# Optimization experiments

Hardware: AMD Instinct MI355X
Metric: run time of the kernel (lower is better)

The kernel has to match this reference:

```python
import jax, jax.numpy as jnp
import numpy as np

B = 64
H_FS = W_FS = 56
IN_DIM, OUT_DIM, NUM_HEADS = 96, 192, 2
HEAD_DIM = OUT_DIM // NUM_HEADS  # 96
STRIDE_Q, STRIDE_KV = (2, 2), (4, 4)
REL_RANGE = 2 * (H_FS // STRIDE_Q[0]) - 1  # 55
LN_EPS = 1e-5


def setup_inputs() -> dict:
    key = jax.random.key(0)
    ks = jax.random.split(key, 12)
    N = H_FS * W_FS + 1  # +1 cls token
    s = 0.02
    d = {
        "hidden_states": jax.random.normal(ks[0], (B, N, IN_DIM), jnp.float32),
        "Wq": jax.random.normal(ks[1], (IN_DIM, OUT_DIM), jnp.float32) * s,
        "bq": jnp.zeros((OUT_DIM,), jnp.float32),
        "Wk": jax.random.normal(ks[2], (IN_DIM, OUT_DIM), jnp.float32) * s,
        "bk": jnp.zeros((OUT_DIM,), jnp.float32),
        "Wv": jax.random.normal(ks[3], (IN_DIM, OUT_DIM), jnp.float32) * s,
        "bv": jnp.zeros((OUT_DIM,), jnp.float32),
        # depthwise pool convs: (C_out=C, C_in/groups=1, kh, kw)
        "pool_q_w": jax.random.normal(ks[4], (IN_DIM, 1, 3, 3), jnp.float32) * 0.1,
        "pool_k_w": jax.random.normal(ks[5], (IN_DIM, 1, 3, 3), jnp.float32) * 0.1,
        "pool_v_w": jax.random.normal(ks[6], (IN_DIM, 1, 3, 3), jnp.float32) * 0.1,
        "gq": jnp.ones((IN_DIM,), jnp.float32), "betaq": jnp.zeros((IN_DIM,), jnp.float32),
        "gk": jnp.ones((IN_DIM,), jnp.float32), "betak": jnp.zeros((IN_DIM,), jnp.float32),
        "gv": jnp.ones((IN_DIM,), jnp.float32), "betav": jnp.zeros((IN_DIM,), jnp.float32),
        "rel_h": jax.random.normal(ks[7], (REL_RANGE, HEAD_DIM), jnp.float32) * s,
        "rel_w": jax.random.normal(ks[8], (REL_RANGE, HEAD_DIM), jnp.float32) * s,
        "height": H_FS,
        "width": W_FS,
    }
    return d


def _layernorm(x, g, b):
    m = x.mean(-1, keepdims=True)
    v = ((x - m) ** 2).mean(-1, keepdims=True)
    return (x - m) * jax.lax.rsqrt(v + LN_EPS) * g + b


def _pool(x, w, stride, g, b, height, width):
    # x: (B, folds=1, N, C) with cls token first
    bsz, _, _, C = x.shape
    cls_tok, rest = x[:, :, :1], x[:, :, 1:]
    sp = rest.reshape(bsz, height, width, C).transpose(0, 3, 1, 2)  # (B, C, H, W)
    y = jax.lax.conv_general_dilated(
        sp, w, stride, [(1, 1), (1, 1)], feature_group_count=C,
        dimension_numbers=("NCHW", "OIHW", "NCHW"))
    hp, wp = y.shape[2], y.shape[3]
    y = y.reshape(bsz, 1, C, hp * wp).transpose(0, 1, 3, 2)  # (B, 1, N', C)
    y = jnp.concatenate([cls_tok, y], axis=2)
    return _layernorm(y, g, b), (hp, wp)


def _rel_idx(qn, kn):
    q_ratio = max(kn / qn, 1.0)
    k_ratio = max(qn / kn, 1.0)
    dist = (np.arange(qn)[:, None] * q_ratio - np.arange(kn)[None, :] * k_ratio
            + (kn - 1) * k_ratio)
    return dist.astype(np.int64)


def reference(hidden_states, Wq, bq, Wk, bk, Wv, bv, pool_q_w, pool_k_w, pool_v_w,
              gq, betaq, gk, betak, gv, betav, rel_h, rel_w, height, width):
    bsz, N, C = hidden_states.shape
    h = hidden_states.reshape(bsz, N, 1, C).transpose(0, 2, 1, 3)  # (B, folds=1, N, C)

    q, (qh, qw) = _pool(h, pool_q_w, STRIDE_Q, gq, betaq, height, width)
    k, (kh, kw) = _pool(h, pool_k_w, STRIDE_KV, gk, betak, height, width)
    v, _ = _pool(h, pool_v_w, STRIDE_KV, gv, betav, height, width)

    def proj(x, W, bias, n):
        x = x.transpose(0, 2, 1, 3).reshape(bsz, n, -1)
        x = x @ W + bias
        return x.reshape(bsz, n, NUM_HEADS, HEAD_DIM).transpose(0, 2, 1, 3)

    nq, nk = qh * qw + 1, kh * kw + 1
    q = proj(q, Wq, bq, nq)  # (B, H, nq, d)
    k = proj(k, Wk, bk, nk)
    v = proj(v, Wv, bv, nk)

    scale = HEAD_DIM ** -0.5
    attn = jnp.einsum("bhqd,bhkd->bhqk", q * scale, k)

    # decomposed spatial relative positional bias (cls offset = 1)
    Rh = rel_h[_rel_idx(qh, kh)]  # (qh, kh, d)
    Rw = rel_w[_rel_idx(qw, kw)]  # (qw, kw, d)
    rq = q[:, :, 1:].reshape(bsz, NUM_HEADS, qh, qw, HEAD_DIM)
    eh = jnp.einsum("byhwc,hkc->byhwk", rq, Rh)
    ew = jnp.einsum("byhwc,wkc->byhwk", rq, Rw)
    blk = (attn[:, :, 1:, 1:].reshape(bsz, NUM_HEADS, qh, qw, kh, kw)
           + eh[..., :, None] + ew[..., None, :])
    attn = attn.at[:, :, 1:, 1:].set(blk.reshape(bsz, NUM_HEADS, qh * qw, kh * kw))

    attn = jax.nn.softmax(attn, axis=-1)
    out = jnp.einsum("bhqk,bhkd->bhqd", attn, v)
    out = out.at[:, :, 1:].add(q[:, :, 1:])  # residual pooling (skip cls)
    return out.transpose(0, 2, 1, 3).reshape(bsz, nq, OUT_DIM)
```

## Files before the change

kernel.cpp:

```cpp
#include <hip/hip_runtime.h>
#include <hip/hip_bf16.h>

#define B_    64
#define HFS   56
#define CIN   96
#define NQ    785
#define NK    197
#define QW    28
#define KW    14
#define NTOT  3137
#define NQP   800
#define NKP   208
#define NKPV  224
#define VROWS 112
#define KSCL  0.10206207261596575f

typedef __attribute__((ext_vector_type(8))) short short8;
typedef __attribute__((ext_vector_type(4))) short shortx4;
typedef __attribute__((ext_vector_type(4))) float floatx4;

__device__ __forceinline__ short f2s(float x) {
    __hip_bfloat16 h = __float2bfloat16(x);
    return *reinterpret_cast<short*>(&h);
}
__device__ __forceinline__ float s2f(short s) {
    __hip_bfloat16 h; *reinterpret_cast<short*>(&h) = s;
    return __bfloat162float(h);
}
__device__ __forceinline__ short8 ld8(const short* p) {
    return *reinterpret_cast<const short8*>(p);
}

#define MFMA16(a,b,c) __builtin_amdgcn_mfma_f32_16x16x32_bf16((a),(b),(c),0,0,0)

__global__ void prep_kernel(const float* __restrict__ Wq, const float* __restrict__ Wk,
                            const float* __restrict__ Wv, const float* __restrict__ relh,
                            const float* __restrict__ relw,
                            const float* __restrict__ pqw, const float* __restrict__ pkw,
                            const float* __restrict__ pvw,
                            short* __restrict__ WTq, short* __restrict__ WTk,
                            short* __restrict__ WTv, short* __restrict__ relc,
                            short* __restrict__ vt,
                            float* __restrict__ cwqT, float* __restrict__ cwkT,
                            float* __restrict__ cwvT)
{
    int i = blockIdx.x * 256 + threadIdx.x;
    if (i < 18432)      { int o = i/96, c = i%96;              WTq[o*96+c] = f2s(Wq[c*192+o]); }
    else if (i < 36864) { int j = i-18432; int o=j/96,c=j%96;  WTk[o*96+c] = f2s(Wk[c*192+o]*KSCL); }
    else if (i < 55296) { int j = i-36864; int o=j/96,c=j%96;  WTv[o*96+c] = f2s(Wv[c*192+o]); }
    else if (i < 66048) {
        int j = i - 55296;  int r = j/96, c = j%96;
        float v = (r < 54) ? relh[r*96+c] : ((r < 108) ? relw[(r-54)*96+c] : 0.f);
        relc[r*96+c] = f2s(v);
    } else if (i < 721408) {
        int j2 = i - 66048;
        int bh = j2 / 5120, r = j2 % 5120;
        int row, tok; short val;
        if (r < 3584) { row = 96 + r/224; tok = r%224;
                        val = (row == 96 && tok < NK) ? (short)0x3F80 : (short)0; }
        else          { int rr = r-3584; row = rr/16; tok = 208 + (rr%16); val = 0; }
        vt[((long)bh*VROWS + row)*NKPV + tok] = val;
    } else if (i < 724000) {
        int j = i - 721408;
        int w = j / 864, r = j % 864;
        int c = r / 9, off = r % 9;
        const float* src = (w == 0) ? pqw : (w == 1) ? pkw : pvw;
        float*       dst = (w == 0) ? cwqT : (w == 1) ? cwkT : cwvT;
        dst[off*96 + c] = src[c*9 + off];
    }
}

__device__ __forceinline__ void ln_store2(float xa, float xb, bool act,
    const float* __restrict__ g, const float* __restrict__ beta,
    short* __restrict__ outp, int c)
{
    float s  = act ? (xa + xb) : 0.f;
    float ss = act ? (xa*xa + xb*xb) : 0.f;
    #pragma unroll
    for (int off = 32; off >= 1; off >>= 1) {
        s  += __shfl_xor(s,  off, 64);
        ss += __shfl_xor(ss, off, 64);
    }
    float m   = s / CIN;
    float var = ss / CIN - m*m;
    float r   = rsqrtf(var + 1e-5f);
    if (act) {
        float2 g2 = *reinterpret_cast<const float2*>(g + c);
        float2 b2 = *reinterpret_cast<const float2*>(beta + c);
        unsigned pa = (unsigned short)f2s((xa - m)*r*g2.x + b2.x);
        unsigned pb = (unsigned short)f2s((xb - m)*r*g2.y + b2.y);
        *reinterpret_cast<unsigned*>(outp + c) = pa | (pb << 16);
    }
}

__global__ __launch_bounds__(256) void pool_ln_kernel(
    const float* __restrict__ hs,
    const float* __restrict__ cwqT, const float* __restrict__ cwkT, const float* __restrict__ cwvT,
    const float* __restrict__ gq, const float* __restrict__ betaq,
    const float* __restrict__ gk, const float* __restrict__ betak,
    const float* __restrict__ gv, const float* __restrict__ betav,
    short* __restrict__ pq, short* __restrict__ pk, short* __restrict__ pv)
{
    int wid  = threadIdx.x >> 6;
    int lane = threadIdx.x & 63;
    int gid  = blockIdx.x * 4 + wid;
    int b = gid / 1008;
    int t = gid % 1008;
    bool act = (lane < 48);
    int c = lane * 2;
    const long hb = (long)b * NTOT * CIN;

    if (t < NQP) {
        short* outp = pq + ((long)b*NQP + t)*CIN;
        if (t >= NQ) { if (act) *reinterpret_cast<unsigned*>(outp + c) = 0u; return; }
        float xa = 0.f, xb = 0.f;
        if (t == 0) {
            if (act) { float2 h2 = *reinterpret_cast<const float2*>(hs + hb + c); xa = h2.x; xb = h2.y; }
        } else {
            int j = t - 1, oy = j / QW, ox = j % QW;
            #pragma unroll
            for (int dy = 0; dy < 3; ++dy) {
                int iy = oy*2 - 1 + dy;
                if (iy < 0 || iy >= HFS) continue;
                #pragma unroll
                for (int dx = 0; dx < 3; ++dx) {
                    int ix = ox*2 - 1 + dx;
                    if (ix < 0 || ix >= HFS) continue;
                    if (act) {
                        long base = hb + (long)(1 + iy*HFS + ix) * CIN;
                        float2 h2 = *reinterpret_cast<const float2*>(hs + base + c);
                        float2 w2 = *reinterpret_cast<const float2*>(cwqT + (dy*3+dx)*96 + c);
                        xa = fmaf(h2.x, w2.x, xa);
                        xb = fmaf(h2.y, w2.y, xb);
                    }
                }
            }
        }
        ln_store2(xa, xb, act, gq, betaq, outp, c);
    } else {
        int tok = t - NQP;
        short* ok_ = pk + ((long)b*NKP + tok)*CIN;
        short* ov_ = pv + ((long)b*NKP + tok)*CIN;
        if (tok >= NK) {
            if (act) {
                *reinterpret_cast<unsigned*>(ok_ + c) = 0u;
                *reinterpret_cast<unsigned*>(ov_ + c) = 0u;
            }
            return;
        }
        float ka = 0.f, kb_ = 0.f, va = 0.f, vb = 0.f;
        if (tok == 0) {
            if (act) {
                float2 h2 = *reinterpret_cast<const float2*>(hs + hb + c);
                ka = va = h2.x;  kb_ = vb = h2.y;
            }
        } else {
            int j = tok - 1, oy = j / KW, ox = j % KW;
            #pragma unroll
            for (int dy = 0; dy < 3; ++dy) {
                int iy = oy*4 - 1 + dy;
                if (iy < 0 || iy >= HFS) continue;
                #pragma unroll
                for (int dx = 0; dx < 3; ++dx) {
                    int ix = ox*4 - 1 + dx;
                    if (ix < 0 || ix >= HFS) continue;
                    if (act) {
                        long base = hb + (long)(1 + iy*HFS + ix) * CIN;
                        int wo = (dy*3+dx)*96 + c;
                        float2 h2 = *reinterpret_cast<const float2*>(hs + base + c);
                        float2 wk2 = *reinterpret_cast<const float2*>(cwkT + wo);
                        float2 wv2 = *reinterpret_cast<const float2*>(cwvT + wo);
                        ka  = fmaf(h2.x, wk2.x, ka);
                        kb_ = fmaf(h2.y, wk2.y, kb_);
                        va  = fmaf(h2.x, wv2.x, va);
                        vb  = fmaf(h2.y, wv2.y, vb);
                    }
                }
            }
        }
        ln_store2(ka, kb_, act, gk, betak, ok_, c);
        ln_store2(va, vb, act, gv, betav, ov_, c);
    }
}

__global__ __launch_bounds__(256) void proj_mfma_kernel(
    const short* __restrict__ pq, const short* __restrict__ pk, const short* __restrict__ pv,
    const short* __restrict__ WTq, const short* __restrict__ WTk, const short* __restrict__ WTv,
    const float* __restrict__ bq, const float* __restrict__ bk, const float* __restrict__ bv,
    short* __restrict__ qb, short* __restrict__ kb, short* __restrict__ vt)
{
    int wid  = threadIdx.x >> 6;
    int lane = threadIdx.x & 63;
    int quad = lane >> 4, col = lane & 15;
    int wt = blockIdx.x * 4 + wid;

    if (wt < 4032) {
        const short *A, *WT; const float* bias; short* outp;
        int ntokp, row0; float bsc;
        if (wt < 3200) { A = pq; WT = WTq; bias = bq; outp = qb; ntokp = NQP; row0 = wt*16; bsc = 1.f; }
        else           { A = pk; WT = WTk; bias = bk; outp = kb; ntokp = NKP; row0 = (wt-3200)*16; bsc = KSCL; }

        short8 bt[3];
        #pragma unroll
        for (int cc = 0; cc < 3; ++cc)
            bt[cc] = ld8(A + (long)(row0 + col)*96 + cc*32 + quad*8);

        int b = row0 / ntokp;
        int tok = (row0 % ntokp) + col;

        #pragma unroll
        for (int nt = 0; nt < 12; ++nt) {
            floatx4 acc = {0.f, 0.f, 0.f, 0.f};
            #pragma unroll
            for (int cc = 0; cc < 3; ++cc) {
                short8 af = ld8(WT + (nt*16 + col)*96 + cc*32 + quad*8);
                acc = MFMA16(af, bt[cc], acc);
            }
            int o0 = nt*16 + quad*4;
            float4 bo = *reinterpret_cast<const float4*>(bias + o0);
            int h  = (o0 >= 96) ? 1 : 0;
            int d0 = o0 - h*96;
            shortx4 val;
            val.x = f2s(acc[0] + bo.x*bsc);
            val.y = f2s(acc[1] + bo.y*bsc);
            val.z = f2s(acc[2] + bo.z*bsc);
            val.w = f2s(acc[3] + bo.w*bsc);
            *reinterpret_cast<shortx4*>(outp + ((long)(b*2 + h)*ntokp + tok)*96 + d0) = val;
        }
    } else {
        int row0 = (wt - 4032) * 16;
        short8 at[3];
        #pragma unroll
        for (int cc = 0; cc < 3; ++cc)
            at[cc] = ld8(pv + (long)(row0 + col)*96 + cc*32 + quad*8);

        int b = row0 / NKP;
        int tloc0 = (row0 % NKP) + quad*4;

        #pragma unroll
        for (int nt = 0; nt < 12; ++nt) {
            floatx4 acc = {0.f, 0.f, 0.f, 0.f};
            #pragma unroll
            for (int cc = 0; cc < 3; ++cc) {
                short8 bf = ld8(WTv + (nt*16 + col)*96 + cc*32 + quad*8);
                acc = MFMA16(at[cc], bf, acc);
            }
            int o = nt*16 + col;
            int h = (o >= 96) ? 1 : 0;
            int d = o - h*96;
            float bo = bv[o];
            shortx4 val;
            val.x = (tloc0+0 < NK) ? f2s(acc[0] + bo) : (short)0;
            val.y = (tloc0+1 < NK) ? f2s(acc[1] + bo) : (short)0;
            val.z = (tloc0+2 < NK) ? f2s(acc[2] + bo) : (short)0;
            val.w = (tloc0+3 < NK) ? f2s(acc[3] + bo) : (short)0;
            *reinterpret_cast<shortx4*>(vt + ((long)(b*2 + h)*VROWS + d)*NKPV + tloc0) = val;
        }
    }
}

__global__ __launch_bounds__(256) void attn_kernel(
    const short* __restrict__ qb, const short* __restrict__ kb,
    const short* __restrict__ vt, const short* __restrict__ relc,
    float* __restrict__ out)
{
    __shared__ short e_s[4][16][112];
    __shared__ __align__(16) short p_s[4][16][232];

    int tid  = threadIdx.x;
    int wid  = tid >> 6;
    int lane = tid & 63;
    int quad = lane >> 4, col = lane & 15;

    int bid = blockIdx.x;
    int tb  = (bid & 7) * 200 + (bid >> 3);
    int wt  = tb * 4 + wid;
    int bh  = wt / 50;
    int t   = wt % 50;
    int q0  = t * 16;

    const short* qrow = qb + ((long)bh*NQP + q0)*96;
    short8 aq[3];
    #pragma unroll
    for (int c = 0; c < 3; ++c)
        aq[c] = ld8(qrow + col*96 + c*32 + quad*8);

    #pragma unroll
    for (int rt = 0; rt < 7; ++rt) {
        floatx4 acc = {0.f, 0.f, 0.f, 0.f};
        #pragma unroll
        for (int c = 0; c < 3; ++c) {
            short8 bf = ld8(relc + (rt*16 + col)*96 + c*32 + quad*8);
            acc = MFMA16(aq[c], bf, acc);
        }
        #pragma unroll
        for (int reg = 0; reg < 4; ++reg)
            e_s[wid][quad*4 + reg][rt*16 + col] = f2s(acc[reg]);
    }

    int qyo[4], qxo[4];
    #pragma unroll
    for (int reg = 0; reg < 4; ++reg) {
        int qq = q0 + quad*4 + reg;
        int jj = (qq > 0) ? (qq - 1) : 0;
        qyo[reg] = jj / QW;
        qxo[reg] = jj % QW;
    }

    const short* kbase = kb + (long)bh*NKP*96;
    #pragma unroll
    for (int kt = 0; kt < 13; ++kt) {
        floatx4 acc = {0.f, 0.f, 0.f, 0.f};
        #pragma unroll
        for (int c = 0; c < 3; ++c) {
            short8 bf = ld8(kbase + (kt*16 + col)*96 + c*32 + quad*8);
            acc = MFMA16(aq[c], bf, acc);
        }
        int k  = kt*16 + col;
        int kk = (k > 0) ? (k - 1) : 0;
        int ky = kk / 14;  ky = (ky < 13) ? ky : 13;
        int kx = kk - 14*ky;
        int oh = 26 - 2*ky;
        int ow2 = 26 - 2*kx;
        #pragma unroll
        for (int reg = 0; reg < 4; ++reg) {
            const short* er = &e_s[wid][quad*4 + reg][0];
            float bias = s2f(er[qyo[reg] + oh]) + s2f(er[54 + qxo[reg] + ow2]);
            if (kt == 0) bias = (col == 0) ? 0.f : bias;
            if (q0 == 0 && reg == 0) bias = (quad == 0) ? 0.f : bias;
            p_s[wid][quad*4 + reg][k] = f2s(__expf(acc[reg] + bias));
        }
    }
    #pragma unroll
    for (int reg = 0; reg < 4; ++reg)
        p_s[wid][quad*4 + reg][208 + col] = 0;

    floatx4 o[7];
    #pragma unroll
    for (int nt = 0; nt < 7; ++nt) o[nt] = floatx4{0.f, 0.f, 0.f, 0.f};
    const short* vbase = vt + (long)bh*VROWS*NKPV;
    #pragma unroll
    for (int c = 0; c < 7; ++c) {
        short8 ap = ld8(&p_s[wid][col][c*32 + quad*8]);
        #pragma unroll
        for (int nt = 0; nt < 7; ++nt) {
            short8 bf = ld8(vbase + (nt*16 + col)*NKPV + c*32 + quad*8);
            o[nt] = MFMA16(ap, bf, o[nt]);
        }
    }

    float inv[4];
    #pragma unroll
    for (int reg = 0; reg < 4; ++reg) {
        float srow = __shfl(o[6][reg], lane & 48, 64);
        inv[reg] = 1.0f / srow;
    }
    int b = bh >> 1, h = bh & 1;
    #pragma unroll
    for (int nt = 0; nt < 6; ++nt) {
        int ch = nt*16 + col;
        #pragma unroll
        for (int reg = 0; reg < 4; ++reg) {
            int q = q0 + quad*4 + reg;
            if (q < NQ) {
                float val = o[nt][reg] * inv[reg];
                if (q > 0) val += s2f(qb[((long)bh*NQP + q)*96 + ch]);
                out[((long)b*NQ + q)*192 + h*96 + ch] = val;
            }
        }
    }
}

extern "C" void kernel_launch(void* const* d_in, const int* in_sizes, int n_in,
                              void* d_out, int out_size, void* d_ws, size_t ws_size,
                              hipStream_t stream)
{
    const float* hs    = (const float*)d_in[0];
    const float* Wq    = (const float*)d_in[1];
    const float* bq    = (const float*)d_in[2];
    const float* Wk    = (const float*)d_in[3];
    const float* bk    = (const float*)d_in[4];
    const float* Wv    = (const float*)d_in[5];
    const float* bv    = (const float*)d_in[6];
    const float* pqw   = (const float*)d_in[7];
    const float* pkw   = (const float*)d_in[8];
    const float* pvw   = (const float*)d_in[9];
    const float* gq    = (const float*)d_in[10];
    const float* betaq = (const float*)d_in[11];
    const float* gk    = (const float*)d_in[12];
    const float* betak = (const float*)d_in[13];
    const float* gv    = (const float*)d_in[14];
    const float* betav = (const float*)d_in[15];
    const float* relh  = (const float*)d_in[16];
    const float* relw  = (const float*)d_in[17];
    float* out = (float*)d_out;

    short* pq   = (short*)d_ws;
    short* pk   = pq  + (long)B_*NQP*CIN;
    short* pv   = pk  + (long)B_*NKP*CIN;
    short* qb   = pv  + (long)B_*NKP*CIN;
    short* kb   = qb  + (long)128*NQP*96;
    short* vt   = kb  + (long)128*NKP*96;
    short* WTq  = vt  + (long)128*VROWS*NKPV;
    short* WTk  = WTq + 192*96;
    short* WTv  = WTk + 192*96;
    short* relc = WTv + 192*96;
    float* cwqT = (float*)(relc + 112*96);
    float* cwkT = cwqT + 9*96;
    float* cwvT = cwkT + 9*96;

    prep_kernel<<<2829, 256, 0, stream>>>(Wq, Wk, Wv, relh, relw,
                                          pqw, pkw, pvw,
                                          WTq, WTk, WTv, relc, vt,
                                          cwqT, cwkT, cwvT);

    pool_ln_kernel<<<(B_*1008)/4, 256, 0, stream>>>(
        hs, cwqT, cwkT, cwvT, gq, betaq, gk, betak, gv, betav, pq, pk, pv);

    proj_mfma_kernel<<<4864/4, 256, 0, stream>>>(
        pq, pk, pv, WTq, WTk, WTv, bq, bk, bv, qb, kb, vt);

    attn_kernel<<<1600, 256, 0, stream>>>(qb, kb, vt, relc, out);
}
```

Before: 276.5 us.

## Fuse pooling+layernorm with QKV projection and shrink attention block shared memory

Merges the pool/layernorm kernel and the projection kernel into one. Each 256-thread block pools and normalizes a 16-token tile into shared memory, then runs the projection MFMAs directly from that tile. This removes the intermediate pq/pk/pv global round trip and one launch, and hoists the conv weights into registers. The attention kernel moves to 128-thread blocks, reuses a single shared buffer for both the positional-bias table and the probabilities, and precomputes per-row bias gather indices to cut LDS use and raise occupancy. The trade-off is that fewer waves now share the projection work per block.

```diff
diff --git a/kernel.cpp b/kernel.cpp
--- a/kernel.cpp
+++ b/kernel.cpp
@@ -70,54 +70,50 @@
     }
 }
 
-__device__ __forceinline__ void ln_store2(float xa, float xb, bool act,
-    const float* __restrict__ g, const float* __restrict__ beta,
-    short* __restrict__ outp, int c)
-{
-    float s  = act ? (xa + xb) : 0.f;
-    float ss = act ? (xa*xa + xb*xb) : 0.f;
-    #pragma unroll
-    for (int off = 32; off >= 1; off >>= 1) {
-        s  += __shfl_xor(s,  off, 64);
-        ss += __shfl_xor(ss, off, 64);
-    }
-    float m   = s / CIN;
-    float var = ss / CIN - m*m;
-    float r   = rsqrtf(var + 1e-5f);
-    if (act) {
-        float2 g2 = *reinterpret_cast<const float2*>(g + c);
-        float2 b2 = *reinterpret_cast<const float2*>(beta + c);
-        unsigned pa = (unsigned short)f2s((xa - m)*r*g2.x + b2.x);
-        unsigned pb = (unsigned short)f2s((xb - m)*r*g2.y + b2.y);
-        *reinterpret_cast<unsigned*>(outp + c) = pa | (pb << 16);
-    }
-}
-
-__global__ __launch_bounds__(256) void pool_ln_kernel(
+__global__ __launch_bounds__(256) void pool_proj_kernel(
     const float* __restrict__ hs,
     const float* __restrict__ cwqT, const float* __restrict__ cwkT, const float* __restrict__ cwvT,
     const float* __restrict__ gq, const float* __restrict__ betaq,
     const float* __restrict__ gk, const float* __restrict__ betak,
     const float* __restrict__ gv, const float* __restrict__ betav,
-    short* __restrict__ pq, short* __restrict__ pk, short* __restrict__ pv)
+    const short* __restrict__ WTq, const short* __restrict__ WTk, const short* __restrict__ WTv,
+    const float* __restrict__ bq, const float* __restrict__ bk, const float* __restrict__ bv,
+    short* __restrict__ qb, short* __restrict__ kb, short* __restrict__ vt)
 {
-    int wid  = threadIdx.x >> 6;
-    int lane = threadIdx.x & 63;
-    int gid  = blockIdx.x * 4 + wid;
-    int b = gid / 1008;
-    int t = gid % 1008;
+    __shared__ short tiles[2][16][96];
+
+    int tid  = threadIdx.x;
+    int w    = tid >> 6;
+    int lane = tid & 63;
+    int quad = lane >> 4, col = lane & 15;
     bool act = (lane < 48);
     int c = lane * 2;
+
+    int blk = blockIdx.x;
+    bool qmode = (blk < 3200);
+    int b, t0;
+    if (qmode) { b = blk / 50; t0 = (blk % 50) * 16; }
+    else       { int r = blk - 3200; b = r / 13; t0 = (r % 13) * 16; }
     const long hb = (long)b * NTOT * CIN;
 
-    if (t < NQP) {
-        short* outp = pq + ((long)b*NQP + t)*CIN;
-        if (t >= NQ) { if (act) *reinterpret_cast<unsigned*>(outp + c) = 0u; return; }
-        float xa = 0.f, xb = 0.f;
-        if (t == 0) {
-            if (act) { float2 h2 = *reinterpret_cast<const float2*>(hs + hb + c); xa = h2.x; xb = h2.y; }
-        } else {
-            int j = t - 1, oy = j / QW, ox = j % QW;
+    if (qmode) {
+        float2 w2[9];
+        if (act) {
+            #pragma unroll
+            for (int o = 0; o < 9; ++o)
+                w2[o] = *reinterpret_cast<const float2*>(cwqT + o*96 + c);
+        }
+        float xa[4], xb[4];
+        #pragma unroll
+        for (int i = 0; i < 4; ++i) {
+            xa[i] = 0.f; xb[i] = 0.f;
+            int tok = t0 + w*4 + i;
+            if (tok >= NQ) continue;
+            if (tok == 0) {
+                if (act) { float2 h2 = *reinterpret_cast<const float2*>(hs + hb + c); xa[i] = h2.x; xb[i] = h2.y; }
+                continue;
+            }
+            int j = tok - 1, oy = j / QW, ox = j % QW;
             #pragma unroll
             for (int dy = 0; dy < 3; ++dy) {
                 int iy = oy*2 - 1 + dy;
@@ -127,34 +123,53 @@
                     int ix = ox*2 - 1 + dx;
                     if (ix < 0 || ix >= HFS) continue;
                     if (act) {
-                        long base = hb + (long)(1 + iy*HFS + ix) * CIN;
-                        float2 h2 = *reinterpret_cast<const float2*>(hs + base + c);
-                        float2 w2 = *reinterpret_cast<const float2*>(cwqT + (dy*3+dx)*96 + c);
-                        xa = fmaf(h2.x, w2.x, xa);
-                        xb = fmaf(h2.y, w2.y, xb);
+                        float2 h2 = *reinterpret_cast<const float2*>(hs + hb + (long)(1 + iy*HFS + ix)*CIN + c);
+                        xa[i] = fmaf(h2.x, w2[dy*3+dx].x, xa[i]);
+                        xb[i] = fmaf(h2.y, w2[dy*3+dx].y, xb[i]);
                     }
                 }
             }
         }
-        ln_store2(xa, xb, act, gq, betaq, outp, c);
+        #pragma unroll
+        for (int i = 0; i < 4; ++i) {
+            int tok = t0 + w*4 + i;
+            int rl  = w*4 + i;
+            if (tok >= NQ) { if (act) *reinterpret_cast<unsigned*>(&tiles[0][rl][c]) = 0u; continue; }
+            float s  = act ? (xa[i] + xb[i]) : 0.f;
+            float ss = act ? (xa[i]*xa[i] + xb[i]*xb[i]) : 0.f;
+            #pragma unroll
+            for (int off = 32; off >= 1; off >>= 1) { s += __shfl_xor(s, off, 64); ss += __shfl_xor(ss, off, 64); }
+            float m = s / CIN, var = ss / CIN - m*m, r = rsqrtf(var + 1e-5f);
+            if (act) {
+                float2 g2 = *reinterpret_cast<const float2*>(gq + c);
+                float2 b2 = *reinterpret_cast<const float2*>(betaq + c);
+                unsigned pa = (unsigned short)f2s((xa[i]-m)*r*g2.x + b2.x);
+                unsigned pb = (unsigned short)f2s((xb[i]-m)*r*g2.y + b2.y);
+                *reinterpret_cast<unsigned*>(&tiles[0][rl][c]) = pa | (pb << 16);
+            }
+        }
     } else {
-        int tok = t - NQP;
-        short* ok_ = pk + ((long)b*NKP + tok)*CIN;
-        short* ov_ = pv + ((long)b*NKP + tok)*CIN;
-        if (tok >= NK) {
-            if (act) {
-                *reinterpret_cast<unsigned*>(ok_ + c) = 0u;
-                *reinterpret_cast<unsigned*>(ov_ + c) = 0u;
-            }
-            return;
-        }
-        float ka = 0.f, kb_ = 0.f, va = 0.f, vb = 0.f;
-        if (tok == 0) {
-            if (act) {
-                float2 h2 = *reinterpret_cast<const float2*>(hs + hb + c);
-                ka = va = h2.x;  kb_ = vb = h2.y;
-            }
-        } else {
+        float2 wk2[9], wv2[9];
+        if (act) {
+            #pragma unroll
+            for (int o = 0; o < 9; ++o) {
+                wk2[o] = *reinterpret_cast<const float2*>(cwkT + o*96 + c);
+                wv2[o] = *reinterpret_cast<const float2*>(cwvT + o*96 + c);
+            }
+        }
+        float ka[4], kb2[4], va[4], vb2[4];
+        #pragma unroll
+        for (int i = 0; i < 4; ++i) {
+            ka[i] = 0.f; kb2[i] = 0.f; va[i] = 0.f; vb2[i] = 0.f;
+            int tok = t0 + w*4 + i;
+            if (tok >= NK) continue;
+            if (tok == 0) {
+                if (act) {
+                    float2 h2 = *reinterpret_cast<const float2*>(hs + hb + c);
+                    ka[i] = va[i] = h2.x;  kb2[i] = vb2[i] = h2.y;
+                }
+                continue;
+            }
             int j = tok - 1, oy = j / KW, ox = j % KW;
             #pragma unroll
             for (int dy = 0; dy < 3; ++dy) {
@@ -165,107 +180,130 @@
                     int ix = ox*4 - 1 + dx;
                     if (ix < 0 || ix >= HFS) continue;
                     if (act) {
-                        long base = hb + (long)(1 + iy*HFS + ix) * CIN;
-                        int wo = (dy*3+dx)*96 + c;
-                        float2 h2 = *reinterpret_cast<const float2*>(hs + base + c);
-                        float2 wk2 = *reinterpret_cast<const float2*>(cwkT + wo);
-                        float2 wv2 = *reinterpret_cast<const float2*>(cwvT + wo);
-                        ka  = fmaf(h2.x, wk2.x, ka);
-                        kb_ = fmaf(h2.y, wk2.y, kb_);
-                        va  = fmaf(h2.x, wv2.x, va);
-                        vb  = fmaf(h2.y, wv2.y, vb);
+                        float2 h2 = *reinterpret_cast<const float2*>(hs + hb + (long)(1 + iy*HFS + ix)*CIN + c);
+                        int o = dy*3 + dx;
+                        ka[i]  = fmaf(h2.x, wk2[o].x, ka[i]);
+                        kb2[i] = fmaf(h2.y, wk2[o].y, kb2[i]);
+                        va[i]  = fmaf(h2.x, wv2[o].x, va[i]);
+                        vb2[i] = fmaf(h2.y, wv2[o].y, vb2[i]);
                     }
                 }
             }
         }
-        ln_store2(ka, kb_, act, gk, betak, ok_, c);
-        ln_store2(va, vb, act, gv, betav, ov_, c);
-    }
-}
-
-__global__ __launch_bounds__(256) void proj_mfma_kernel(
-    const short* __restrict__ pq, const short* __restrict__ pk, const short* __restrict__ pv,
-    const short* __restrict__ WTq, const short* __restrict__ WTk, const short* __restrict__ WTv,
-    const float* __restrict__ bq, const float* __restrict__ bk, const float* __restrict__ bv,
-    short* __restrict__ qb, short* __restrict__ kb, short* __restrict__ vt)
-{
-    int wid  = threadIdx.x >> 6;
-    int lane = threadIdx.x & 63;
-    int quad = lane >> 4, col = lane & 15;
-    int wt = blockIdx.x * 4 + wid;
-
-    if (wt < 4032) {
-        const short *A, *WT; const float* bias; short* outp;
-        int ntokp, row0; float bsc;
-        if (wt < 3200) { A = pq; WT = WTq; bias = bq; outp = qb; ntokp = NQP; row0 = wt*16; bsc = 1.f; }
-        else           { A = pk; WT = WTk; bias = bk; outp = kb; ntokp = NKP; row0 = (wt-3200)*16; bsc = KSCL; }
-
+        #pragma unroll
+        for (int i = 0; i < 4; ++i) {
+            int tok = t0 + w*4 + i;
+            int rl  = w*4 + i;
+            if (tok >= NK) {
+                if (act) {
+                    *reinterpret_cast<unsigned*>(&tiles[0][rl][c]) = 0u;
+                    *reinterpret_cast<unsigned*>(&tiles[1][rl][c]) = 0u;
+                }
+                continue;
+            }
+            float s1  = act ? (ka[i] + kb2[i]) : 0.f;
+            float ss1 = act ? (ka[i]*ka[i] + kb2[i]*kb2[i]) : 0.f;
+            float s2  = act ? (va[i] + vb2[i]) : 0.f;
+            float ss2 = act ? (va[i]*va[i] + vb2[i]*vb2[i]) : 0.f;
+            #pragma unroll
+            for (int off = 32; off >= 1; off >>= 1) {
+                s1 += __shfl_xor(s1, off, 64); ss1 += __shfl_xor(ss1, off, 64);
+                s2 += __shfl_xor(s2, off, 64); ss2 += __shfl_xor(ss2, off, 64);
+            }
+            float m1 = s1 / CIN, r1 = rsqrtf(ss1/CIN - m1*m1 + 1e-5f);
+            float m2 = s2 / CIN, r2 = rsqrtf(ss2/CIN - m2*m2 + 1e-5f);
+            if (act) {
+                float2 gk2 = *reinterpret_cast<const float2*>(gk + c);
+                float2 bk2 = *reinterpret_cast<const float2*>(betak + c);
+                float2 gv2 = *reinterpret_cast<const float2*>(gv + c);
+                float2 bv2 = *reinterpret_cast<const float2*>(betav + c);
+                unsigned pa = (unsigned short)f2s((ka[i]-m1)*r1*gk2.x + bk2.x);
+                unsigned pb = (unsigned short)f2s((kb2[i]-m1)*r1*gk2.y + bk2.y);
+                *reinterpret_cast<unsigned*>(&tiles[0][rl][c]) = pa | (pb << 16);
+                pa = (unsigned short)f2s((va[i]-m2)*r2*gv2.x + bv2.x);
+                pb = (unsigned short)f2s((vb2[i]-m2)*r2*gv2.y + bv2.y);
+                *reinterpret_cast<unsigned*>(&tiles[1][rl][c]) = pa | (pb << 16);
+            }
+        }
+    }
+    __syncthreads();
+
+    if (qmode) {
         short8 bt[3];
         #pragma unroll
         for (int cc = 0; cc < 3; ++cc)
-            bt[cc] = ld8(A + (long)(row0 + col)*96 + cc*32 + quad*8);
-
-        int b = row0 / ntokp;
-        int tok = (row0 % ntokp) + col;
-
-        #pragma unroll
-        for (int nt = 0; nt < 12; ++nt) {
+            bt[cc] = ld8(&tiles[0][col][cc*32 + quad*8]);
+        int tok = t0 + col;
+        #pragma unroll
+        for (int m2 = 0; m2 < 3; ++m2) {
+            int nt = w*3 + m2;
             floatx4 acc = {0.f, 0.f, 0.f, 0.f};
             #pragma unroll
             for (int cc = 0; cc < 3; ++cc) {
-                short8 af = ld8(WT + (nt*16 + col)*96 + cc*32 + quad*8);
+                short8 af = ld8(WTq + (nt*16 + col)*96 + cc*32 + quad*8);
                 acc = MFMA16(af, bt[cc], acc);
             }
             int o0 = nt*16 + quad*4;
-            float4 bo = *reinterpret_cast<const float4*>(bias + o0);
-            int h  = (o0 >= 96) ? 1 : 0;
+            float4 bo = *reinterpret_cast<const float4*>(bq + o0);
+            int h = (o0 >= 96) ? 1 : 0;
             int d0 = o0 - h*96;
             shortx4 val;
-            val.x = f2s(acc[0] + bo.x*bsc);
-            val.y = f2s(acc[1] + bo.y*bsc);
-            val.z = f2s(acc[2] + bo.z*bsc);
-            val.w = f2s(acc[3] + bo.w*bsc);
-            *reinterpret_cast<shortx4*>(outp + ((long)(b*2 + h)*ntokp + tok)*96 + d0) = val;
+            val.x = f2s(acc[0] + bo.x); val.y = f2s(acc[1] + bo.y);
+            val.z = f2s(acc[2] + bo.z); val.w = f2s(acc[3] + bo.w);
+            *reinterpret_cast<shortx4*>(qb + ((long)(b*2 + h)*NQP + tok)*96 + d0) = val;
         }
     } else {
-        int row0 = (wt - 4032) * 16;
-        short8 at[3];
-        #pragma unroll
-        for (int cc = 0; cc < 3; ++cc)
-            at[cc] = ld8(pv + (long)(row0 + col)*96 + cc*32 + quad*8);
-
-        int b = row0 / NKP;
-        int tloc0 = (row0 % NKP) + quad*4;
-
-        #pragma unroll
-        for (int nt = 0; nt < 12; ++nt) {
+        short8 btk[3], atv[3];
+        #pragma unroll
+        for (int cc = 0; cc < 3; ++cc) {
+            btk[cc] = ld8(&tiles[0][col][cc*32 + quad*8]);
+            atv[cc] = ld8(&tiles[1][col][cc*32 + quad*8]);
+        }
+        int tok = t0 + col;
+        int tl0 = t0 + quad*4;
+        #pragma unroll
+        for (int m2 = 0; m2 < 3; ++m2) {
+            int nt = w*3 + m2;
             floatx4 acc = {0.f, 0.f, 0.f, 0.f};
+            #pragma unroll
+            for (int cc = 0; cc < 3; ++cc) {
+                short8 af = ld8(WTk + (nt*16 + col)*96 + cc*32 + quad*8);
+                acc = MFMA16(af, btk[cc], acc);
+            }
+            int o0 = nt*16 + quad*4;
+            float4 bo = *reinterpret_cast<const float4*>(bk + o0);
+            int h = (o0 >= 96) ? 1 : 0;
+            int d0 = o0 - h*96;
+            shortx4 val;
+            val.x = f2s(acc[0] + bo.x*KSCL); val.y = f2s(acc[1] + bo.y*KSCL);
+            val.z = f2s(acc[2] + bo.z*KSCL); val.w = f2s(acc[3] + bo.w*KSCL);
+            *reinterpret_cast<shortx4*>(kb + ((long)(b*2 + h)*NKP + tok)*96 + d0) = val;
+            floatx4 acc2 = {0.f, 0.f, 0.f, 0.f};
             #pragma unroll
             for (int cc = 0; cc < 3; ++cc) {
                 short8 bf = ld8(WTv + (nt*16 + col)*96 + cc*32 + quad*8);
-                acc = MFMA16(at[cc], bf, acc);
+                acc2 = MFMA16(atv[cc], bf, acc2);
             }
             int o = nt*16 + col;
-            int h = (o >= 96) ? 1 : 0;
-            int d = o - h*96;
-            float bo = bv[o];
-            shortx4 val;
-            val.x = (tloc0+0 < NK) ? f2s(acc[0] + bo) : (short)0;
-            val.y = (tloc0+1 < NK) ? f2s(acc[1] + bo) : (short)0;
-            val.z = (tloc0+2 < NK) ? f2s(acc[2] + bo) : (short)0;
-            val.w = (tloc0+3 < NK) ? f2s(acc[3] + bo) : (short)0;
-            *reinterpret_cast<shortx4*>(vt + ((long)(b*2 + h)*VROWS + d)*NKPV + tloc0) = val;
-        }
-    }
-}
-
-__global__ __launch_bounds__(256) void attn_kernel(
+            int h2 = (o >= 96) ? 1 : 0;
+            int d = o - h2*96;
+            float bo1 = bv[o];
+            shortx4 vv;
+            vv.x = (tl0+0 < NK) ? f2s(acc2[0] + bo1) : (short)0;
+            vv.y = (tl0+1 < NK) ? f2s(acc2[1] + bo1) : (short)0;
+            vv.z = (tl0+2 < NK) ? f2s(acc2[2] + bo1) : (short)0;
+            vv.w = (tl0+3 < NK) ? f2s(acc2[3] + bo1) : (short)0;
+            *reinterpret_cast<shortx4*>(vt + ((long)(b*2 + h2)*VROWS + d)*NKPV + tl0) = vv;
+        }
+    }
+}
+
+__global__ __launch_bounds__(128) void attn_kernel(
     const short* __restrict__ qb, const short* __restrict__ kb,
     const short* __restrict__ vt, const short* __restrict__ relc,
     float* __restrict__ out)
 {
-    __shared__ short e_s[4][16][112];
-    __shared__ __align__(16) short p_s[4][16][232];
+    __shared__ short buf[2][16][260];
 
     int tid  = threadIdx.x;
     int wid  = tid >> 6;
@@ -273,11 +311,12 @@
     int quad = lane >> 4, col = lane & 15;
 
     int bid = blockIdx.x;
-    int tb  = (bid & 7) * 200 + (bid >> 3);
-    int wt  = tb * 4 + wid;
+    int tb  = (bid & 7) * 400 + (bid >> 3);
+    int wt  = tb * 2 + wid;
     int bh  = wt / 50;
     int t   = wt % 50;
     int q0  = t * 16;
+    short (*W)[260] = buf[wid];
 
     const short* qrow = qb + ((long)bh*NQP + q0)*96;
     short8 aq[3];
@@ -295,16 +334,21 @@
         }
         #pragma unroll
         for (int reg = 0; reg < 4; ++reg)
-            e_s[wid][quad*4 + reg][rt*16 + col] = f2s(acc[reg]);
-    }
-
-    int qyo[4], qxo[4];
-    #pragma unroll
-    for (int reg = 0; reg < 4; ++reg) {
-        int qq = q0 + quad*4 + reg;
-        int jj = (qq > 0) ? (qq - 1) : 0;
-        qyo[reg] = jj / QW;
-        qxo[reg] = jj % QW;
+            W[quad*4 + reg][rt*16 + col] = f2s(acc[reg]);
+    }
+
+    {
+        int grow = lane & 15;
+        int gq2  = q0 + grow;
+        int gj0  = (gq2 > 0) ? (gq2 - 1) : 0;
+        int gqy  = gj0 / QW, gqx = gj0 % QW;
+        int jb   = (lane >> 4) * 7;
+        #pragma unroll
+        for (int u = 0; u < 7; ++u) {
+            int j = jb + u;
+            int idx = (j < 14) ? (gqy - 2*j + 26) : (54 + gqx - 2*(j-14) + 26);
+            W[grow][232 + j] = W[grow][idx];
+        }
     }
 
     const short* kbase = kb + (long)bh*NKP*96;
@@ -320,20 +364,18 @@
         int kk = (k > 0) ? (k - 1) : 0;
         int ky = kk / 14;  ky = (ky < 13) ? ky : 13;
         int kx = kk - 14*ky;
-        int oh = 26 - 2*ky;
-        int ow2 = 26 - 2*kx;
         #pragma unroll
         for (int reg = 0; reg < 4; ++reg) {
-            const short* er = &e_s[wid][quad*4 + reg][0];
-            float bias = s2f(er[qyo[reg] + oh]) + s2f(er[54 + qxo[reg] + ow2]);
+            int row = quad*4 + reg;
+            float bias = s2f(W[row][232 + ky]) + s2f(W[row][246 + kx]);
             if (kt == 0) bias = (col == 0) ? 0.f : bias;
             if (q0 == 0 && reg == 0) bias = (quad == 0) ? 0.f : bias;
-            p_s[wid][quad*4 + reg][k] = f2s(__expf(acc[reg] + bias));
+            W[row][k] = f2s(__expf(acc[reg] + bias));
         }
     }
     #pragma unroll
     for (int reg = 0; reg < 4; ++reg)
-        p_s[wid][quad*4 + reg][208 + col] = 0;
+        W[quad*4 + reg][208 + col] = 0;
 
     floatx4 o[7];
     #pragma unroll
@@ -341,7 +383,7 @@
     const short* vbase = vt + (long)bh*VROWS*NKPV;
     #pragma unroll
     for (int c = 0; c < 7; ++c) {
-        short8 ap = ld8(&p_s[wid][col][c*32 + quad*8]);
+        short8 ap = ld8(&W[col][c*32 + quad*8]);
         #pragma unroll
         for (int nt = 0; nt < 7; ++nt) {
             short8 bf = ld8(vbase + (nt*16 + col)*NKPV + c*32 + quad*8);
@@ -395,10 +437,7 @@
     const float* relw  = (const float*)d_in[17];
     float* out = (float*)d_out;
 
-    short* pq   = (short*)d_ws;
-    short* pk   = pq  + (long)B_*NQP*CIN;
-    short* pv   = pk  + (long)B_*NKP*CIN;
-    short* qb   = pv  + (long)B_*NKP*CIN;
+    short* qb   = (short*)d_ws;
     short* kb   = qb  + (long)128*NQP*96;
     short* vt   = kb  + (long)128*NKP*96;
     short* WTq  = vt  + (long)128*VROWS*NKPV;
@@ -414,11 +453,9 @@
                                           WTq, WTk, WTv, relc, vt,
                                           cwqT, cwkT, cwvT);
 
-    pool_ln_kernel<<<(B_*1008)/4, 256, 0, stream>>>(
-        hs, cwqT, cwkT, cwvT, gq, betaq, gk, betak, gv, betav, pq, pk, pv);
-
-    proj_mfma_kernel<<<4864/4, 256, 0, stream>>>(
-        pq, pk, pv, WTq, WTk, WTv, bq, bk, bv, qb, kb, vt);
-
-    attn_kernel<<<1600, 256, 0, stream>>>(qb, kb, vt, relc, out);
-}
+    pool_proj_kernel<<<4032, 256, 0, stream>>>(
+        hs, cwqT, cwkT, cwvT, gq, betaq, gk, betak, gv, betav,
+        WTq, WTk, WTv, bq, bk, bv, qb, kb, vt);
+
+    attn_kernel<<<3200, 128, 0, stream>>>(qb, kb, vt, relc, out);
+}
```

Measured after the change: 293.9 us. 1.06x slower.
